# Optimization experiments

Measured on AMD Instinct MI355X. Metric: run time of the kernel, lower is better.

## Reference

```python
import jax, jax.numpy as jnp
import numpy as np

B = 65536
D = 512
R = 64  # min(64, D) reflections (cap_householder_refl=True)


def setup_inputs() -> dict:
    key = jax.random.key(0)
    k1, k2 = jax.random.split(key)
    x = jax.random.normal(k1, (B, D), dtype=jnp.float32)
    sldj = jnp.zeros((B,), dtype=jnp.float32)
    householder_params = jax.random.normal(k2, (D, R), dtype=jnp.float32)
    return {"x": x, "sldj": sldj, "householder_params": householder_params}


def reference(x, sldj, householder_params):
    # Sequential Householder reflections: x <- x - 2 (x . u_hat) u_hat
    # params: (D, R); unconditioned, so u is shared across the batch.
    us = householder_params.T  # (R, D), scanned in forward order i = 0..R-1

    def step(xc, u):
        unit_u = u / jnp.linalg.norm(u)          # (D,)
        scalar = xc @ unit_u                      # (B,)
        xc = xc - 2.0 * scalar[:, None] * unit_u  # rank-1 update
        return xc, None

    out, _ = jax.lax.scan(step, x, us)
    return out, sldj
```

## Files before the change

### kernel.cpp

```cpp
#include <hip/hip_runtime.h>

typedef __attribute__((ext_vector_type(8))) short bf16x8;
typedef __attribute__((ext_vector_type(4))) float f32x4;

#define DD 512
#define RR 64
#define BTOT 65536
#define BM 128
#define BN 128
#define BK 32

static __device__ __forceinline__ unsigned short f2bf(float f) {
    union { float f; unsigned u; } v; v.f = f;
    unsigned r = v.u + 0x7fffu + ((v.u >> 16) & 1u);
    return (unsigned short)(r >> 16);
}

__global__ void normalize_kernel(const float* __restrict__ P, float* __restrict__ U) {
    int i = blockIdx.x;
    int t = threadIdx.x;
    __shared__ float red[4];
    float a = P[t * RR + i];
    float b = P[(t + 256) * RR + i];
    float p = a * a + b * b;
#pragma unroll
    for (int off = 32; off > 0; off >>= 1) p += __shfl_down(p, off);
    if ((t & 63) == 0) red[t >> 6] = p;
    __syncthreads();
    float s = red[0] + red[1] + red[2] + red[3];
    float inv = 1.0f / sqrtf(s);
    U[i * DD + t]       = a * inv;
    U[i * DD + t + 256] = b * inv;
}

__global__ void compose_kernel(const float* __restrict__ U, unsigned short* __restrict__ Mt) {
    int kb = blockIdx.x * 4;
    int t = threadIdx.x;
    int w = t >> 6;
    __shared__ float red[2][4][4];
    float v0[4], v1[4];
#pragma unroll
    for (int c = 0; c < 4; ++c) {
        v0[c] = (kb + c == t) ? 1.0f : 0.0f;
        v1[c] = (kb + c == t + 256) ? 1.0f : 0.0f;
    }
    float u0n = U[t], u1n = U[t + 256];
    for (int i = 0; i < RR; ++i) {
        float u0 = u0n, u1 = u1n;
        if (i + 1 < RR) { u0n = U[(i + 1) * DD + t]; u1n = U[(i + 1) * DD + t + 256]; }
        float p0 = v0[0] * u0 + v1[0] * u1;
        float p1 = v0[1] * u0 + v1[1] * u1;
        float p2 = v0[2] * u0 + v1[2] * u1;
        float p3 = v0[3] * u0 + v1[3] * u1;
#pragma unroll
        for (int off = 32; off > 0; off >>= 1) {
            p0 += __shfl_down(p0, off);
            p1 += __shfl_down(p1, off);
            p2 += __shfl_down(p2, off);
            p3 += __shfl_down(p3, off);
        }
        if ((t & 63) == 0) {
            red[i & 1][w][0] = p0; red[i & 1][w][1] = p1;
            red[i & 1][w][2] = p2; red[i & 1][w][3] = p3;
        }
        __syncthreads();
        float d[4];
#pragma unroll
        for (int c = 0; c < 4; ++c)
            d[c] = red[i & 1][0][c] + red[i & 1][1][c] + red[i & 1][2][c] + red[i & 1][3][c];
#pragma unroll
        for (int c = 0; c < 4; ++c) {
            v0[c] -= 2.0f * d[c] * u0;
            v1[c] -= 2.0f * d[c] * u1;
        }
    }
#pragma unroll
    for (int c = 0; c < 4; ++c) {
        Mt[(size_t)t * DD + kb + c]         = f2bf(v0[c]);
        Mt[(size_t)(t + 256) * DD + kb + c] = f2bf(v1[c]);
    }
}

__launch_bounds__(256, 4)
__global__ void gemm_kernel(const float* __restrict__ X,
                            const unsigned short* __restrict__ Mt,
                            float* __restrict__ out) {
    __shared__ __attribute__((aligned(16))) float lAf[BM * BK];
    __shared__ __attribute__((aligned(16))) unsigned short lB[BN * BK];

    int t = threadIdx.x;
    int wave = t >> 6, lane = t & 63;
    int wm = wave >> 1, wn = wave & 1;
    int quad = lane >> 4, l16 = lane & 15;
    int row0 = (int)(blockIdx.x >> 2) * BM;
    int col0 = (int)(blockIdx.x & 3) * BN;

    f32x4 acc[4][4] = {};

    int a_kg = (lane & 7) ^ (lane >> 3);
    int a_mrow = wave * 32 + (lane >> 3);
    int b_kg = (lane & 3) ^ ((lane >> 2) & 3);
    int b_nrow = wave * 32 + (lane >> 2);

    const float* aBase = X + (size_t)(row0 + a_mrow) * DD + a_kg * 4;
    const unsigned short* bBase = Mt + (size_t)(col0 + b_nrow) * DD + b_kg * 8;

#pragma unroll 1
    for (int k0 = 0; k0 < DD; k0 += BK) {
#pragma unroll
        for (int q = 0; q < 4; ++q) {
            const float* g = aBase + k0 + (size_t)q * 8 * DD;
            __builtin_amdgcn_global_load_lds(
                (const __attribute__((address_space(1))) unsigned int*)g,
                (__attribute__((address_space(3))) unsigned int*)(lAf + (wave * 32 + q * 8) * BK),
                16, 0, 0);
        }
#pragma unroll
        for (int q = 0; q < 2; ++q) {
            const unsigned short* g = bBase + k0 + (size_t)q * 16 * DD;
            __builtin_amdgcn_global_load_lds(
                (const __attribute__((address_space(1))) unsigned int*)g,
                (__attribute__((address_space(3))) unsigned int*)(lB + (wave * 32 + q * 16) * BK),
                16, 0, 0);
        }
        __syncthreads();

        bf16x8 bfr[4];
#pragma unroll
        for (int nt = 0; nt < 4; ++nt) {
            int n = wn * 64 + nt * 16 + l16;
            bfr[nt] = *(const bf16x8*)(lB + n * BK + (quad ^ (l16 & 3)) * 8);
        }
#pragma unroll
        for (int mt = 0; mt < 4; ++mt) {
            int m = wm * 64 + mt * 16 + l16;
            int s0 = (2 * quad) ^ (l16 & 7);
            int s1 = (2 * quad + 1) ^ (l16 & 7);
            float4 fa0 = *(const float4*)(lAf + m * BK + s0 * 4);
            float4 fa1 = *(const float4*)(lAf + m * BK + s1 * 4);
            bf16x8 afr;
            afr[0] = (short)f2bf(fa0.x); afr[1] = (short)f2bf(fa0.y);
            afr[2] = (short)f2bf(fa0.z); afr[3] = (short)f2bf(fa0.w);
            afr[4] = (short)f2bf(fa1.x); afr[5] = (short)f2bf(fa1.y);
            afr[6] = (short)f2bf(fa1.z); afr[7] = (short)f2bf(fa1.w);
#pragma unroll
            for (int nt = 0; nt < 4; ++nt)
                acc[mt][nt] = __builtin_amdgcn_mfma_f32_16x16x32_bf16(afr, bfr[nt], acc[mt][nt], 0, 0, 0);
        }
        __syncthreads();
    }

#pragma unroll
    for (int mt = 0; mt < 4; ++mt) {
#pragma unroll
        for (int r = 0; r < 4; ++r) {
            int row = row0 + wm * 64 + mt * 16 + quad * 4 + r;
            float* orow = out + (size_t)row * DD + col0 + wn * 64 + l16;
#pragma unroll
            for (int nt = 0; nt < 4; ++nt)
                orow[nt * 16] = acc[mt][nt][r];
        }
    }
}

__global__ void sldj_kernel(const float4* __restrict__ s, float4* __restrict__ o) {
    int i = blockIdx.x * blockDim.x + threadIdx.x;
    o[i] = s[i];
}

extern "C" void kernel_launch(void* const* d_in, const int* in_sizes, int n_in,
                              void* d_out, int out_size, void* d_ws, size_t ws_size,
                              hipStream_t stream) {
    const float* x      = (const float*)d_in[0];
    const float* sldj   = (const float*)d_in[1];
    const float* params = (const float*)d_in[2];
    float* out = (float*)d_out;

    float* U = (float*)d_ws;
    unsigned short* Mt = (unsigned short*)((char*)d_ws + RR * DD * sizeof(float));

    normalize_kernel<<<RR, 256, 0, stream>>>(params, U);
    compose_kernel<<<DD / 4, 256, 0, stream>>>(U, Mt);
    gemm_kernel<<<(BTOT / BM) * (DD / BN), 256, 0, stream>>>(x, Mt, out);
    sldj_kernel<<<BTOT / 4 / 256, 256, 0, stream>>>((const float4*)sldj,
                                                    (float4*)(out + (size_t)BTOT * DD));
}
```

Baseline: 304.2 us.

## Fuse sldj copy into GEMM, swizzle block order, use cheaper bf16 packing

Folds the sldj copy into the first 64 GEMM blocks, which removes one kernel launch. Block indices are remapped so groups of 8 row tiles share column tiles, aiming for better L2 reuse of X rows across the four column blocks. The per-element round-to-nearest-even bf16 conversion is replaced with a round-half-up add followed by a single byte-permute that packs two values at once, cutting ALU work in the inner loop. The rounding now differs slightly from round-to-nearest-even.

```diff
diff --git a/kernel.cpp b/kernel.cpp
--- a/kernel.cpp
+++ b/kernel.cpp
@@ -14,6 +14,13 @@
     union { float f; unsigned u; } v; v.f = f;
     unsigned r = v.u + 0x7fffu + ((v.u >> 16) & 1u);
     return (unsigned short)(r >> 16);
+}
+
+static __device__ __forceinline__ unsigned pack2bf(float x, float y) {
+    union { float f; unsigned u; } a, b;
+    a.f = x; b.f = y;
+    unsigned ax = a.u + 0x8000u, bx = b.u + 0x8000u;
+    return __builtin_amdgcn_perm(bx, ax, 0x07060302u);
 }
 
 __global__ void normalize_kernel(const float* __restrict__ P, float* __restrict__ U) {
@@ -84,16 +91,28 @@
 __launch_bounds__(256, 4)
 __global__ void gemm_kernel(const float* __restrict__ X,
                             const unsigned short* __restrict__ Mt,
+                            const float* __restrict__ sldj,
                             float* __restrict__ out) {
     __shared__ __attribute__((aligned(16))) float lAf[BM * BK];
     __shared__ __attribute__((aligned(16))) unsigned short lB[BN * BK];
 
     int t = threadIdx.x;
+    int bid = blockIdx.x;
+
+    if (bid < 64) {
+        const float4* s4 = (const float4*)sldj;
+        float4* o4 = (float4*)(out + (size_t)BTOT * DD);
+        o4[bid * 256 + t] = s4[bid * 256 + t];
+    }
+
+    int row_t = (bid >> 5) * 8 + (bid & 7);
+    int col_t = (bid >> 3) & 3;
+    int row0 = row_t * BM;
+    int col0 = col_t * BN;
+
     int wave = t >> 6, lane = t & 63;
     int wm = wave >> 1, wn = wave & 1;
     int quad = lane >> 4, l16 = lane & 15;
-    int row0 = (int)(blockIdx.x >> 2) * BM;
-    int col0 = (int)(blockIdx.x & 3) * BN;
 
     f32x4 acc[4][4] = {};
 
@@ -138,14 +157,14 @@
             int s1 = (2 * quad + 1) ^ (l16 & 7);
             float4 fa0 = *(const float4*)(lAf + m * BK + s0 * 4);
             float4 fa1 = *(const float4*)(lAf + m * BK + s1 * 4);
-            bf16x8 afr;
-            afr[0] = (short)f2bf(fa0.x); afr[1] = (short)f2bf(fa0.y);
-            afr[2] = (short)f2bf(fa0.z); afr[3] = (short)f2bf(fa0.w);
-            afr[4] = (short)f2bf(fa1.x); afr[5] = (short)f2bf(fa1.y);
-            afr[6] = (short)f2bf(fa1.z); afr[7] = (short)f2bf(fa1.w);
+            union { unsigned u[4]; bf16x8 v; } afr;
+            afr.u[0] = pack2bf(fa0.x, fa0.y);
+            afr.u[1] = pack2bf(fa0.z, fa0.w);
+            afr.u[2] = pack2bf(fa1.x, fa1.y);
+            afr.u[3] = pack2bf(fa1.z, fa1.w);
 #pragma unroll
             for (int nt = 0; nt < 4; ++nt)
-                acc[mt][nt] = __builtin_amdgcn_mfma_f32_16x16x32_bf16(afr, bfr[nt], acc[mt][nt], 0, 0, 0);
+                acc[mt][nt] = __builtin_amdgcn_mfma_f32_16x16x32_bf16(afr.v, bfr[nt], acc[mt][nt], 0, 0, 0);
         }
         __syncthreads();
     }
@@ -163,11 +182,6 @@
     }
 }
 
-__global__ void sldj_kernel(const float4* __restrict__ s, float4* __restrict__ o) {
-    int i = blockIdx.x * blockDim.x + threadIdx.x;
-    o[i] = s[i];
-}
-
 extern "C" void kernel_launch(void* const* d_in, const int* in_sizes, int n_in,
                               void* d_out, int out_size, void* d_ws, size_t ws_size,
                               hipStream_t stream) {
@@ -181,7 +195,5 @@
 
     normalize_kernel<<<RR, 256, 0, stream>>>(params, U);
     compose_kernel<<<DD / 4, 256, 0, stream>>>(U, Mt);
-    gemm_kernel<<<(BTOT / BM) * (DD / BN), 256, 0, stream>>>(x, Mt, out);
-    sldj_kernel<<<BTOT / 4 / 256, 256, 0, stream>>>((const float4*)sldj,
-                                                    (float4*)(out + (size_t)BTOT * DD));
+    gemm_kernel<<<(BTOT / BM) * (DD / BN), 256, 0, stream>>>(x, Mt, sldj, out);
 }
```

Measured after the change: 298.1 us. -2.0%, faster.
